# Performance work log

Hardware: AMD Instinct MI355X
Metric: run time of the kernel (lower is better)

## Reference

```python
import jax, jax.numpy as jnp
import numpy as np

BN_EPS = 1e-3          # nn.BatchNorm1d(..., eps=0.001)
NUM_PILLARS = 600000   # M = total occupied pillars across the batch
N_POINTS = 3_000_000
C_IN, C_OUT = 10, 64


def setup_inputs() -> dict:
    key = jax.random.key(0)
    k1, k2, k3 = jax.random.split(key, 3)
    pts_feature = jax.random.normal(k1, (N_POINTS, C_IN), dtype=jnp.float32)
    point_pillar_indices = jax.random.randint(k2, (N_POINTS,), 0, NUM_PILLARS, dtype=jnp.int32)
    # Linear(C_IN, C_OUT, bias=False), kaiming_normal init
    W = jax.random.normal(k3, (C_IN, C_OUT), dtype=jnp.float32) * np.sqrt(2.0 / C_IN)
    # BatchNorm1d in eval mode (running stats)
    gamma = jnp.ones((C_OUT,), jnp.float32)
    beta = jnp.zeros((C_OUT,), jnp.float32)
    run_mean = jnp.zeros((C_OUT,), jnp.float32)
    run_var = jnp.ones((C_OUT,), jnp.float32)
    return {"pts_feature": pts_feature, "point_pillar_indices": point_pillar_indices,
            "W": W, "gamma": gamma, "beta": beta, "run_mean": run_mean, "run_var": run_var}


def reference(pts_feature, point_pillar_indices, W, gamma, beta, run_mean, run_var):
    # shared MLP: Linear(no bias) -> BatchNorm1d(eval) -> ReLU, fused per-point
    h = pts_feature @ W                                        # (N, C_OUT)
    h = gamma * (h - run_mean) * jax.lax.rsqrt(run_var + BN_EPS) + beta
    h = jax.nn.relu(h)
    # scatter_max over irregular pillar ids -> (M, C_OUT)
    pooled = jax.ops.segment_max(h, point_pillar_indices, num_segments=NUM_PILLARS)
    # torch scatter_max leaves empty pillars at 0; jax gives -inf -> replace
    return jnp.where(jnp.isfinite(pooled), pooled, 0.0)
```

## Files before the change

kernel.cpp:

```cpp
#include <hip/hip_runtime.h>
#include <hip/hip_bf16.h>

#define C_IN 10
#define C_OUT 64
#define BN_EPS 1e-3f

#define BPF   256
#define CB    256
#define NBMAX 4704
#define TS    2048
#define MAXT  2048

typedef __attribute__((ext_vector_type(8))) short bf16x8;
typedef __attribute__((ext_vector_type(4))) float f32x4;


__global__ __launch_bounds__(1024) void k1_hist(const int* __restrict__ idx, int n, int chunk,
                                                unsigned* __restrict__ ghist, int NB, int shift) {
    __shared__ unsigned h[NBMAX];
    const int b = blockIdx.x, t = threadIdx.x;
    for (int i = t; i < NB; i += 1024) h[i] = 0u;
    __syncthreads();
    const int lo = b * chunk;
    const int hi = min(n, lo + chunk);
    for (int i = lo + t; i < hi; i += 1024)
        atomicAdd(&h[((unsigned)idx[i]) >> shift], 1u);
    __syncthreads();
    for (int k = t; k < NB; k += 1024) ghist[(size_t)k * CB + b] = h[k];
}

__global__ __launch_bounds__(256) void k2a_reduce(const unsigned* __restrict__ g, int G,
                                                  unsigned* __restrict__ tsum) {
    __shared__ unsigned s[256];
    const int t = threadIdx.x;
    const int base = blockIdx.x * TS + t * 8;
    unsigned acc = 0;
#pragma unroll
    for (int j = 0; j < 8; ++j) { int gi = base + j; if (gi < G) acc += g[gi]; }
    s[t] = acc; __syncthreads();
    for (int off = 128; off > 0; off >>= 1) { if (t < off) s[t] += s[t + off]; __syncthreads(); }
    if (t == 0) tsum[blockIdx.x] = s[0];
}

__global__ __launch_bounds__(256) void k2b_scan(unsigned* __restrict__ tsum, int nt) {
    __shared__ unsigned partial[256], basev[256];
    const int t = threadIdx.x;
    const int per = (nt + 255) / 256;
    const int lo = t * per, hi = min(nt, lo + per);
    unsigned s = 0;
    for (int i = lo; i < hi; ++i) s += tsum[i];
    partial[t] = s; __syncthreads();
    if (t == 0) { unsigned a = 0; for (int k = 0; k < 256; ++k) { basev[k] = a; a += partial[k]; } }
    __syncthreads();
    unsigned a = basev[t];
    for (int i = lo; i < hi; ++i) { unsigned v = tsum[i]; tsum[i] = a; a += v; }
}

__global__ __launch_bounds__(256) void k2c_apply(unsigned* __restrict__ g, int G,
                                                 const unsigned* __restrict__ tsum,
                                                 unsigned* __restrict__ bstart, int NB, int n) {
    __shared__ unsigned s[256];
    const int t = threadIdx.x;
    const int base = blockIdx.x * TS + t * 8;
    unsigned v[8]; unsigned acc = 0;
#pragma unroll
    for (int j = 0; j < 8; ++j) { int gi = base + j; v[j] = (gi < G) ? g[gi] : 0u; acc += v[j]; }
    s[t] = acc; __syncthreads();
    for (int off = 1; off < 256; off <<= 1) {
        unsigned x = (t >= off) ? s[t - off] : 0u; __syncthreads();
        s[t] += x; __syncthreads();
    }
    unsigned excl = ((t == 0) ? 0u : s[t - 1]) + tsum[blockIdx.x];
#pragma unroll
    for (int j = 0; j < 8; ++j) {
        int gi = base + j;
        if (gi < G) {
            g[gi] = excl;
            if ((gi & (CB - 1)) == 0) bstart[gi / CB] = excl;
            excl += v[j];
        }
    }
    if (blockIdx.x == 0 && t == 0) bstart[NB] = (unsigned)n;
}

__global__ __launch_bounds__(1024) void k3_scatter(const int* __restrict__ idx, int n, int chunk,
                                                   const unsigned* __restrict__ scanned,
                                                   unsigned* __restrict__ rec, int NB,
                                                   int shift, unsigned lpmask) {
    __shared__ unsigned cnt[NBMAX];
    __shared__ unsigned basel[NBMAX];
    const int b = blockIdx.x, t = threadIdx.x;
    for (int k = t; k < NB; k += 1024) { basel[k] = scanned[(size_t)k * CB + b]; cnt[k] = 0u; }
    __syncthreads();
    const int lo = b * chunk, hi = min(n, lo + chunk);
    for (int i = lo + t; i < hi; i += 1024) {
        unsigned pid = (unsigned)idx[i];
        unsigned k = pid >> shift;
        unsigned r = atomicAdd(&cnt[k], 1u);
        rec[basel[k] + r] = ((pid & lpmask) << 22) | (unsigned)i;
    }
}

static __device__ __forceinline__ unsigned pk2(float2 v) {
    __hip_bfloat162 h = __float22bfloat162_rn(v);
    return *reinterpret_cast<unsigned*>(&h);
}

__global__ __launch_bounds__(1024) void pool_sfm_kernel(
    const float* __restrict__ pts,
    const unsigned* __restrict__ rec,
    const unsigned* __restrict__ bstart,
    const float* __restrict__ W,
    const float* __restrict__ gamma, const float* __restrict__ beta,
    const float* __restrict__ mean, const float* __restrict__ var,
    float* __restrict__ out, int M)
{
    __shared__ unsigned smax[BPF * C_OUT];
    __shared__ unsigned short ord[MAXT + 16];
    __shared__ unsigned lps32[(MAXT + 16) / 4];
    __shared__ unsigned cnt[BPF];
    __shared__ unsigned cur[BPF];
    unsigned char* lpsb = (unsigned char*)lps32;

    const int b = blockIdx.x, t = threadIdx.x;
    const int lane = t & 63, w = t >> 6;
    const int g = lane >> 4, c0 = lane & 15;

    {
        uint4* s4 = (uint4*)smax;
        const uint4 z = make_uint4(0u, 0u, 0u, 0u);
        for (int i = t; i < BPF * C_OUT / 4; i += 1024) s4[i] = z;
    }
    if (t < BPF) cnt[t] = 0u;

    bf16x8 bfrag[4];
#pragma unroll
    for (int tc = 0; tc < 4; ++tc) {
        const int ch = 16 * tc + c0;
        const float sc = gamma[ch] * rsqrtf(var[ch] + BN_EPS);
        const float sh = fmaf(-mean[ch], sc, beta[ch]);
        union { bf16x8 v; unsigned short u[8]; } B;
#pragma unroll
        for (int j = 0; j < 8; ++j) {
            const int k = g * 8 + j;
            float val = 0.f;
            if (k < 10) val = W[k * C_OUT + ch] * sc;
            else if (k == 10) val = sh;
            __hip_bfloat16 hb = __float2bfloat16(val);
            B.u[j] = *reinterpret_cast<unsigned short*>(&hb);
        }
        bfrag[tc] = B.v;
    }

    const unsigned base = bstart[b];
    const int T  = (int)(bstart[b + 1] - base);
    const int Tc = T < MAXT ? T : MAXT;
    __syncthreads();

    int l0i = -1, l1i = -1;
    if (t < Tc)        { l0i = (int)(rec[base + t] >> 22);        atomicAdd(&cnt[l0i], 1u); }
    if (t + 1024 < Tc) { l1i = (int)(rec[base + t + 1024] >> 22); atomicAdd(&cnt[l1i], 1u); }
    __syncthreads();
    if (t < BPF) cur[t] = cnt[t];
    __syncthreads();
    for (int off = 1; off < BPF; off <<= 1) {
        unsigned x = 0;
        if (t < BPF && t >= off) x = cur[t - off];
        __syncthreads();
        if (t < BPF) cur[t] += x;
        __syncthreads();
    }
    if (t < BPF) cur[t] -= cnt[t];
    __syncthreads();
    if (l0i >= 0) { unsigned p = atomicAdd(&cur[l0i], 1u); ord[p] = (unsigned short)t;          lpsb[p] = (unsigned char)l0i; }
    if (l1i >= 0) { unsigned p = atomicAdd(&cur[l1i], 1u); ord[p] = (unsigned short)(t + 1024); lpsb[p] = (unsigned char)l1i; }
    __syncthreads();
    const int nt16 = (Tc + 15) >> 4;
    {
        const int padn = nt16 * 16 - Tc;
        if (Tc > 0 && t < padn) { ord[Tc + t] = ord[Tc - 1]; lpsb[Tc + t] = lpsb[Tc - 1]; }
    }
    __syncthreads();

    for (int tile = w; tile < nt16; tile += 16) {
        const int tb = tile << 4;
        const int o = (int)ord[tb + c0];
        const unsigned rc = rec[base + o];
        const float2* fp = (const float2*)(pts + (size_t)(rc & 0x3FFFFFu) * C_IN);
        uint4 Aq;
        if (g == 0) {
            float2 x0 = fp[0], x1 = fp[1], x2 = fp[2], x3 = fp[3];
            Aq = make_uint4(pk2(x0), pk2(x1), pk2(x2), pk2(x3));
        } else if (g == 1) {
            float2 x4 = fp[4];
            Aq = make_uint4(pk2(x4), 0x00003F80u, 0u, 0u);
        } else {
            Aq = make_uint4(0u, 0u, 0u, 0u);
        }
        union { uint4 q; bf16x8 v; } A; A.q = Aq;

        const unsigned L = *(const unsigned*)(lpsb + tb + (g << 2));

        const f32x4 z4 = {0.f, 0.f, 0.f, 0.f};
        f32x4 a0 = __builtin_amdgcn_mfma_f32_16x16x32_bf16(A.v, bfrag[0], z4, 0, 0, 0);
        f32x4 a1 = __builtin_amdgcn_mfma_f32_16x16x32_bf16(A.v, bfrag[1], z4, 0, 0, 0);
        f32x4 a2 = __builtin_amdgcn_mfma_f32_16x16x32_bf16(A.v, bfrag[2], z4, 0, 0, 0);
        f32x4 a3 = __builtin_amdgcn_mfma_f32_16x16x32_bf16(A.v, bfrag[3], z4, 0, 0, 0);

        const int lp0 = (int)(L & 255u), lp1 = (int)((L >> 8) & 255u),
                  lp2 = (int)((L >> 16) & 255u), lp3 = (int)((L >> 24) & 255u);
        float m0 = a0[0], m1 = a1[0], m2 = a2[0], m3 = a3[0];
        int cp = lp0;
#define FLUSHM() { \
        unsigned* rowp = &smax[((unsigned)cp) << 6]; \
        const unsigned rb = (unsigned)(c0 + cp); \
        atomicMax(&rowp[(rb      ) & 63u], __float_as_uint(fmaxf(m0, 0.f))); \
        atomicMax(&rowp[(rb + 16u) & 63u], __float_as_uint(fmaxf(m1, 0.f))); \
        atomicMax(&rowp[(rb + 32u) & 63u], __float_as_uint(fmaxf(m2, 0.f))); \
        atomicMax(&rowp[(rb + 48u) & 63u], __float_as_uint(fmaxf(m3, 0.f))); }
        if (lp1 == cp) { m0 = fmaxf(m0, a0[1]); m1 = fmaxf(m1, a1[1]); m2 = fmaxf(m2, a2[1]); m3 = fmaxf(m3, a3[1]); }
        else { FLUSHM(); m0 = a0[1]; m1 = a1[1]; m2 = a2[1]; m3 = a3[1]; cp = lp1; }
        if (lp2 == cp) { m0 = fmaxf(m0, a0[2]); m1 = fmaxf(m1, a1[2]); m2 = fmaxf(m2, a2[2]); m3 = fmaxf(m3, a3[2]); }
        else { FLUSHM(); m0 = a0[2]; m1 = a1[2]; m2 = a2[2]; m3 = a3[2]; cp = lp2; }
        if (lp3 == cp) { m0 = fmaxf(m0, a0[3]); m1 = fmaxf(m1, a1[3]); m2 = fmaxf(m2, a2[3]); m3 = fmaxf(m3, a3[3]); }
        else { FLUSHM(); m0 = a0[3]; m1 = a1[3]; m2 = a2[3]; m3 = a3[3]; cp = lp3; }
        FLUSHM();
#undef FLUSHM
    }
    __syncthreads();

    for (int row = w; row < BPF; row += 16) {
        const int gp = b * BPF + row;
        if (gp < M)
            out[(size_t)gp * C_OUT + lane] = __uint_as_float(smax[row * 64 + ((lane + row) & 63)]);
    }

    if (T > MAXT) {
        __syncthreads();
        for (int r = MAXT + w; r < T; r += 16) {
            const unsigned rc = rec[base + r];
            const float* fp = pts + (size_t)(rc & 0x3FFFFFu) * C_IN;
            float h = 0.f;
#pragma unroll
            for (int j = 0; j < C_IN; ++j) h = fmaf(fp[j], W[j * C_OUT + lane], h);
            const float sc = gamma[lane] * rsqrtf(var[lane] + BN_EPS);
            h = fmaxf(fmaf(h, sc, fmaf(-mean[lane], sc, beta[lane])), 0.f);
            const int gp = b * BPF + (int)(rc >> 22);
            atomicMax((unsigned*)&out[(size_t)gp * C_OUT + lane], __float_as_uint(h));
        }
    }
}

__global__ __launch_bounds__(256) void zero_out_kernel(float4* __restrict__ out4, int n4) {
    int i = blockIdx.x * blockDim.x + threadIdx.x;
    int stride = gridDim.x * blockDim.x;
    float4 z = make_float4(0.f, 0.f, 0.f, 0.f);
    for (int j = i; j < n4; j += stride) out4[j] = z;
}

__global__ __launch_bounds__(256) void pillar_scatter_kernel(
    const float* __restrict__ pts, const int* __restrict__ idx,
    const float* __restrict__ W, const float* __restrict__ gamma,
    const float* __restrict__ beta, const float* __restrict__ mean,
    const float* __restrict__ var, unsigned int* __restrict__ out, int npoints)
{
    const int lane = threadIdx.x & 63;
    float wv[C_IN];
#pragma unroll
    for (int j = 0; j < C_IN; ++j) wv[j] = W[j * C_OUT + lane];
    const float scale = gamma[lane] * rsqrtf(var[lane] + BN_EPS);
    const float shift = fmaf(-mean[lane], scale, beta[lane]);
    const int wave_id = (blockIdx.x * blockDim.x + threadIdx.x) >> 6;
    const int nwaves  = (gridDim.x * blockDim.x) >> 6;
    for (int p = wave_id; p < npoints; p += nwaves) {
        const float* f = pts + (size_t)p * C_IN;
        float h = 0.f;
#pragma unroll
        for (int j = 0; j < C_IN; ++j) h = fmaf(f[j], wv[j], h);
        h = fmaxf(fmaf(h, scale, shift), 0.f);
        atomicMax(&out[(size_t)idx[p] * C_OUT + lane], __float_as_uint(h));
    }
}


extern "C" void kernel_launch(void* const* d_in, const int* in_sizes, int n_in,
                              void* d_out, int out_size, void* d_ws, size_t ws_size,
                              hipStream_t stream) {
    const float* pts   = (const float*)d_in[0];
    const int*   idx   = (const int*)  d_in[1];
    const float* W     = (const float*)d_in[2];
    const float* gamma = (const float*)d_in[3];
    const float* beta  = (const float*)d_in[4];
    const float* mean  = (const float*)d_in[5];
    const float* var   = (const float*)d_in[6];

    const int npoints = in_sizes[0] / C_IN;
    const int M       = out_size / C_OUT;
    const int NB      = (M + BPF - 1) / BPF;
    const int G       = NB * CB;
    const int nt      = (G + TS - 1) / TS;
    const int chunk   = (npoints + CB - 1) / CB;

    const size_t head_u32 = (size_t)G + (size_t)nt + (size_t)NB + 1;
    const size_t head_b   = ((head_u32 * 4) + 63) & ~(size_t)63;
    const size_t need     = head_b + (size_t)npoints * 4;

    if (NB <= NBMAX && npoints < (1 << 22) && nt <= 65535 && ws_size >= need) {
        unsigned* ghist  = (unsigned*)d_ws;
        unsigned* tsum   = ghist + G;
        unsigned* bstart = tsum + nt;
        unsigned* rec    = (unsigned*)((char*)d_ws + head_b);

        k1_hist        <<<CB, 1024, 0, stream>>>(idx, npoints, chunk, ghist, NB, 8);
        k2a_reduce     <<<nt, 256,  0, stream>>>(ghist, G, tsum);
        k2b_scan       <<<1,  256,  0, stream>>>(tsum, nt);
        k2c_apply      <<<nt, 256,  0, stream>>>(ghist, G, tsum, bstart, NB, npoints);
        k3_scatter     <<<CB, 1024, 0, stream>>>(idx, npoints, chunk, ghist, rec, NB, 8, 255u);
        pool_sfm_kernel<<<NB, 1024, 0, stream>>>(pts, rec, bstart, W, gamma, beta,
                                                 mean, var, (float*)d_out, M);
        return;
    }

    zero_out_kernel<<<2048, 256, 0, stream>>>((float4*)d_out, out_size / 4);
    pillar_scatter_kernel<<<2048, 256, 0, stream>>>(
        pts, idx, W, gamma, beta, mean, var, (unsigned int*)d_out, npoints);
}
```

Baseline: 206.8 us.

## Software-pipeline point gathers across tiles and use wave-shuffle prefix scan

Replaces the shared-memory Hillis-Steele scan over per-pillar counts with a wavefront shuffle scan plus a small cross-wave fixup, which removes many block-wide barriers. The per-tile loop now prefetches the next tile's point features and the record index two tiles ahead, so dependent global gather latency overlaps with the MFMA and atomicMax work of the current tile. This costs extra registers per thread at 1024 threads per block, which may limit occupancy.

```diff
diff --git a/kernel.cpp b/kernel.cpp
--- a/kernel.cpp
+++ b/kernel.cpp
@@ -120,6 +120,7 @@
     __shared__ unsigned lps32[(MAXT + 16) / 4];
     __shared__ unsigned cnt[BPF];
     __shared__ unsigned cur[BPF];
+    __shared__ unsigned wsum[4];
     unsigned char* lpsb = (unsigned char*)lps32;
 
     const int b = blockIdx.x, t = threadIdx.x;
@@ -161,16 +162,26 @@
     if (t < Tc)        { l0i = (int)(rec[base + t] >> 22);        atomicAdd(&cnt[l0i], 1u); }
     if (t + 1024 < Tc) { l1i = (int)(rec[base + t + 1024] >> 22); atomicAdd(&cnt[l1i], 1u); }
     __syncthreads();
-    if (t < BPF) cur[t] = cnt[t];
-    __syncthreads();
-    for (int off = 1; off < BPF; off <<= 1) {
-        unsigned x = 0;
-        if (t < BPF && t >= off) x = cur[t - off];
-        __syncthreads();
-        if (t < BPF) cur[t] += x;
-        __syncthreads();
-    }
-    if (t < BPF) cur[t] -= cnt[t];
+    unsigned myv = 0, mys = 0;
+    if (t < BPF) {
+        myv = cnt[t];
+        mys = myv;
+#pragma unroll
+        for (int off = 1; off < 64; off <<= 1) {
+            unsigned y = (unsigned)__shfl_up((int)mys, off);
+            if (lane >= off) mys += y;
+        }
+        if (lane == 63) wsum[t >> 6] = mys;
+    }
+    __syncthreads();
+    if (t < BPF) {
+        unsigned add = 0;
+        const int mw = t >> 6;
+        if (mw > 0) add += wsum[0];
+        if (mw > 1) add += wsum[1];
+        if (mw > 2) add += wsum[2];
+        cur[t] = mys - myv + add;
+    }
     __syncthreads();
     if (l0i >= 0) { unsigned p = atomicAdd(&cur[l0i], 1u); ord[p] = (unsigned short)t;          lpsb[p] = (unsigned char)l0i; }
     if (l1i >= 0) { unsigned p = atomicAdd(&cur[l1i], 1u); ord[p] = (unsigned short)(t + 1024); lpsb[p] = (unsigned char)l1i; }
@@ -182,21 +193,42 @@
     }
     __syncthreads();
 
-    for (int tile = w; tile < nt16; tile += 16) {
+    int tile = w;
+    unsigned rcB = 0u;
+    float2 x0p, x1p, x2p, x3p, x4p;
+    x0p = x1p = x2p = x3p = x4p = make_float2(0.f, 0.f);
+    if (tile < nt16) {
+        const int o = (int)ord[(tile << 4) + c0];
+        const unsigned rcA = rec[base + o];
+        const float2* fp = (const float2*)(pts + (size_t)(rcA & 0x3FFFFFu) * C_IN);
+        if (g == 0)      { x0p = fp[0]; x1p = fp[1]; x2p = fp[2]; x3p = fp[3]; }
+        else if (g == 1) { x4p = fp[4]; }
+    }
+    if (tile + 16 < nt16) {
+        const int o = (int)ord[((tile + 16) << 4) + c0];
+        rcB = rec[base + o];
+    }
+
+    for (; tile < nt16; tile += 16) {
         const int tb = tile << 4;
-        const int o = (int)ord[tb + c0];
-        const unsigned rc = rec[base + o];
-        const float2* fp = (const float2*)(pts + (size_t)(rc & 0x3FFFFFu) * C_IN);
+        const float2 x0 = x0p, x1 = x1p, x2 = x2p, x3 = x3p, x4 = x4p;
+
+        unsigned rcC = 0u;
+        if (tile + 32 < nt16) {
+            const int o = (int)ord[((tile + 32) << 4) + c0];
+            rcC = rec[base + o];
+        }
+        if (tile + 16 < nt16) {
+            const float2* fp = (const float2*)(pts + (size_t)(rcB & 0x3FFFFFu) * C_IN);
+            if (g == 0)      { x0p = fp[0]; x1p = fp[1]; x2p = fp[2]; x3p = fp[3]; }
+            else if (g == 1) { x4p = fp[4]; }
+        }
+        rcB = rcC;
+
         uint4 Aq;
-        if (g == 0) {
-            float2 x0 = fp[0], x1 = fp[1], x2 = fp[2], x3 = fp[3];
-            Aq = make_uint4(pk2(x0), pk2(x1), pk2(x2), pk2(x3));
-        } else if (g == 1) {
-            float2 x4 = fp[4];
-            Aq = make_uint4(pk2(x4), 0x00003F80u, 0u, 0u);
-        } else {
-            Aq = make_uint4(0u, 0u, 0u, 0u);
-        }
+        if (g == 0)      Aq = make_uint4(pk2(x0), pk2(x1), pk2(x2), pk2(x3));
+        else if (g == 1) Aq = make_uint4(pk2(x4), 0x00003F80u, 0u, 0u);
+        else             Aq = make_uint4(0u, 0u, 0u, 0u);
         union { uint4 q; bf16x8 v; } A; A.q = Aq;
 
         const unsigned L = *(const unsigned*)(lpsb + tb + (g << 2));
```

After: 202.5 us. 2.1% less time.
